# Optimization experiments

Hardware: AMD Instinct MI355X
Metric: run time of the kernel (lower is better)

## Reference

```python
import jax, jax.numpy as jnp
import numpy as np

REG = 0.1
EPS = 2.220446049250313e-16  # np.finfo(float).eps, cast to working dtype


def setup_inputs() -> dict:
    key = jax.random.key(0)
    k1, k2, k3 = jax.random.split(key, 3)
    x = jax.random.normal(k1, (262144, 512), dtype=jnp.float32)
    w = jax.random.normal(k2, (512,), dtype=jnp.float32)
    b = jax.random.normal(k3, (1,), dtype=jnp.float32)
    return {"x": x, "w": w, "b": b}


def reference(x, w, b):
    # net(x): [N, D] @ [D] + b -> [N]
    out = x @ w + b[0]
    n = out.shape[0]
    # sum(pdist(out[:, None], p=1)) == sum over i<j of |out_i - out_j|.
    # Exact sort-based closed form: with s sorted ascending,
    #   sum_{i<j}(s_j - s_i) = sum_i (2i - (n-1)) * s_i
    s = jnp.sort(out)
    coef = 2.0 * jnp.arange(n, dtype=out.dtype) - jnp.asarray(n - 1, out.dtype)
    pair_sum = jnp.sum(coef * s)
    loss = -jnp.sum(out) + (REG / n) * pair_sum
    # heaviside(out, zero_pos=True) = relu(sign(out + eps)); prod -> verified flag
    is_verified = jnp.prod(jax.nn.relu(jnp.sign(out + jnp.asarray(EPS, out.dtype))))
    return loss, is_verified
```

## Files before the change

### kernel.cpp

```cpp
#include <hip/hip_runtime.h>
#include <stdint.h>
#include <stddef.h>

#define NBINS 65536
#define EPSF 2.220446049250313e-16f
#define RTILE 4096

__device__ __forceinline__ uint32_t f2key(float f) {
    uint32_t u = __float_as_uint(f);
    return (u & 0x80000000u) ? ~u : (u | 0x80000000u);
}
__device__ __forceinline__ float key2f(uint32_t k) {
    uint32_t u = (k & 0x80000000u) ? (k ^ 0x80000000u) : ~k;
    return __uint_as_float(u);
}

__global__ __launch_bounds__(256) void gemv_kernel(
    const float* __restrict__ x, const float* __restrict__ w,
    const float* __restrict__ bptr, uint32_t* __restrict__ keys,
    uint32_t* __restrict__ hist, int N, int D,
    double* __restrict__ sum_out, int* __restrict__ bad_flag)
{
    __shared__ float4 w4s[512];
    const int tid = threadIdx.x;
    const int nf4 = D >> 2;
    const float4* w4g = (const float4*)w;
    for (int i = tid; i < nf4; i += 256) w4s[i] = w4g[i];
    __syncthreads();

    const int wave = tid >> 6, lane = tid & 63;
    const int gwave = blockIdx.x * 4 + wave;
    const int nwaves = gridDim.x * 4;
    const int rows_per = (N + nwaves - 1) / nwaves;
    const int r0 = gwave * rows_per;
    const int r1 = (r0 + rows_per < N) ? (r0 + rows_per) : N;
    const float b0 = bptr[0];

    double lsum = 0.0;
    int lbad = 0;
    for (int row = r0; row < r1; ++row) {
        const float4* xr = (const float4*)(x + (size_t)row * D);
        float dot = 0.f;
        for (int i = lane; i < nf4; i += 64) {
            float4 a = xr[i];
            float4 bb = w4s[i];
            dot = fmaf(a.x, bb.x, dot);
            dot = fmaf(a.y, bb.y, dot);
            dot = fmaf(a.z, bb.z, dot);
            dot = fmaf(a.w, bb.w, dot);
        }
        #pragma unroll
        for (int off = 32; off > 0; off >>= 1) dot += __shfl_down(dot, off, 64);
        if (lane == 0) {
            float f = dot + b0;
            uint32_t k = f2key(f);
            keys[row] = k;
            atomicAdd(&hist[k >> 16], 1u);
            lsum += (double)f;
            lbad |= (f + EPSF > 0.f) ? 0 : 1;
        }
    }

    __shared__ double sd[4];
    __shared__ int si[4];
    if (lane == 0) { sd[wave] = lsum; si[wave] = lbad; }
    __syncthreads();
    if (tid == 0) {
        atomicAdd(sum_out, sd[0] + sd[1] + sd[2] + sd[3]);
        int bd = si[0] | si[1] | si[2] | si[3];
        if (bd) atomicOr(bad_flag, 1);
    }
}

__global__ __launch_bounds__(1024) void scan_kernel(
    const uint32_t* __restrict__ hist, uint32_t* __restrict__ base,
    uint32_t* __restrict__ cnt, uint32_t* __restrict__ nzb,
    int* __restrict__ nb_count)
{
    __shared__ uint32_t partial[1024];
    __shared__ int nb_lds;
    const int t = threadIdx.x;
    if (t == 0) nb_lds = 0;
    const int per = NBINS / 1024;
    uint32_t s = 0;
    for (int i = 0; i < per; ++i) s += hist[t * per + i];
    partial[t] = s;
    __syncthreads();
    for (int off = 1; off < 1024; off <<= 1) {
        uint32_t v = (t >= off) ? partial[t - off] : 0u;
        __syncthreads();
        partial[t] += v;
        __syncthreads();
    }
    uint32_t run = (t == 0) ? 0u : partial[t - 1];
    for (int i = 0; i < per; ++i) {
        int idx = t * per + i;
        uint32_t h = hist[idx];
        base[idx] = run;
        cnt[idx] = run;
        if (h != 0u) {
            int pos = atomicAdd(&nb_lds, 1);
            nzb[pos] = (uint32_t)idx;
        }
        run += h;
    }
    if (t == 1023) base[NBINS] = run;
    __syncthreads();
    if (t == 0) *nb_count = nb_lds;
}

__global__ __launch_bounds__(256) void scatter_kernel(
    const uint32_t* __restrict__ keys, uint32_t* __restrict__ cnt,
    uint32_t* __restrict__ sorted, int N)
{
    int i = blockIdx.x * 256 + threadIdx.x;
    if (i < N) {
        uint32_t k = keys[i];
        uint32_t pos = atomicAdd(&cnt[k >> 16], 1u);
        sorted[pos] = k;
    }
}

__global__ __launch_bounds__(256) void rank_kernel(
    const uint32_t* __restrict__ sorted, const uint32_t* __restrict__ base,
    const uint32_t* __restrict__ nzb, const int* __restrict__ nb_count,
    int N, double* __restrict__ pair_acc, const double* __restrict__ sum_out,
    const int* __restrict__ bad_flag, int* __restrict__ done_cnt,
    float* __restrict__ out)
{
    __shared__ uint32_t tile[RTILE];
    __shared__ double sred[256];
    const int tid = threadIdx.x;
    const int nb = *nb_count;
    double acc = 0.0;

    for (int ib = blockIdx.x; ib < nb; ib += gridDim.x) {
        const uint32_t b = nzb[ib];
        const uint32_t start = base[b], end = base[b + 1];
        const uint32_t m = end - start;

        if (m <= RTILE) {
            __syncthreads();
            for (uint32_t j = tid; j < m; j += 256u) tile[j] = sorted[start + j];
            __syncthreads();
            const uint32_t rounds = (m + 255u) / 256u;
            for (uint32_t r = 0; r < rounds; ++r) {
                uint32_t p = r * 256u + (uint32_t)tid;
                if (p < m) {
                    uint32_t k = tile[p];
                    uint32_t lc = 0, eq = 0;
                    uint32_t m4 = m & ~3u, j = 0;
                    for (; j < m4; j += 4) {
                        uint4 t4 = *(const uint4*)(tile + j);
                        lc += (t4.x < k); eq += (t4.x == k);
                        lc += (t4.y < k); eq += (t4.y == k);
                        lc += (t4.z < k); eq += (t4.z == k);
                        lc += (t4.w < k); eq += (t4.w == k);
                    }
                    for (; j < m; ++j) {
                        uint32_t kk = tile[j];
                        lc += (kk < k); eq += (kk == k);
                    }
                    double coef = 2.0 * (double)(start + lc) + (double)eq - (double)N;
                    acc += coef * (double)key2f(k);
                }
            }
        } else {
            const uint32_t rounds = (m + 255u) / 256u;
            for (uint32_t r = 0; r < rounds; ++r) {
                uint32_t p = start + r * 256u + (uint32_t)tid;
                bool active = (p < end);
                uint32_t k = active ? sorted[p] : 0u;
                uint32_t lc = 0, eq = 0;
                for (uint32_t ts = start; ts < end; ts += RTILE) {
                    uint32_t tn = end - ts;
                    if (tn > RTILE) tn = RTILE;
                    __syncthreads();
                    for (uint32_t j = tid; j < tn; j += 256u) tile[j] = sorted[ts + j];
                    __syncthreads();
                    if (active) {
                        for (uint32_t j = 0; j < tn; ++j) {
                            uint32_t kk = tile[j];
                            lc += (kk < k); eq += (kk == k);
                        }
                    }
                }
                if (active) {
                    double coef = 2.0 * (double)(start + lc) + (double)eq - (double)N;
                    acc += coef * (double)key2f(k);
                }
            }
        }
    }

    sred[tid] = acc;
    __syncthreads();
    for (int off = 128; off > 0; off >>= 1) {
        if (tid < off) sred[tid] += sred[tid + off];
        __syncthreads();
    }
    if (tid == 0) {
        if (sred[0] != 0.0) atomicAdd(pair_acc, sred[0]);
        __threadfence();
        int d = atomicAdd(done_cnt, 1);
        if (d == (int)gridDim.x - 1) {
            __threadfence();
            double pp = __longlong_as_double(
                atomicAdd((unsigned long long*)pair_acc, 0ULL));
            double so = __longlong_as_double(
                atomicAdd((unsigned long long*)const_cast<double*>(sum_out), 0ULL));
            int bd = atomicAdd(const_cast<int*>(bad_flag), 0);
            double loss = -so + (0.1 / (double)N) * pp;
            out[0] = (float)loss;
            out[1] = bd ? 0.0f : 1.0f;
        }
    }
}

extern "C" void kernel_launch(void* const* d_in, const int* in_sizes, int n_in,
                              void* d_out, int out_size, void* d_ws, size_t ws_size,
                              hipStream_t stream) {
    (void)n_in; (void)out_size; (void)ws_size;
    const float* x = (const float*)d_in[0];
    const float* w = (const float*)d_in[1];
    const float* b = (const float*)d_in[2];
    float* out = (float*)d_out;
    const int D = in_sizes[1];
    const int N = in_sizes[0] / D;

    uint8_t* W = (uint8_t*)d_ws;
    uint32_t* hist     = (uint32_t*)(W);
    double*   sum_out  = (double*)(W + 262144);
    double*   pair_acc = (double*)(W + 262152);
    int*      bad_flag = (int*)(W + 262160);
    int*      done_cnt = (int*)(W + 262164);
    int*      nb_count = (int*)(W + 262168);
    uint32_t* base     = (uint32_t*)(W + 262176);
    uint32_t* cnt      = (uint32_t*)(W + 524336);
    uint32_t* nzb      = (uint32_t*)(W + 786480);
    uint32_t* keys     = (uint32_t*)(W + 1048624);
    uint32_t* sorted   = keys + N;

    hipMemsetAsync(d_ws, 0, 262176, stream);
    gemv_kernel<<<2048, 256, 0, stream>>>(x, w, b, keys, hist, N, D, sum_out, bad_flag);
    scan_kernel<<<1, 1024, 0, stream>>>(hist, base, cnt, nzb, nb_count);
    scatter_kernel<<<(N + 255) / 256, 256, 0, stream>>>(keys, cnt, sorted, N);
    rank_kernel<<<2048, 256, 0, stream>>>(sorted, base, nzb, nb_count, N,
                                          pair_acc, sum_out, bad_flag, done_cnt, out);
}
```

Baseline: 985.5 us.

## Parallelize histogram scan across 256 blocks using coarse top-byte counts

The gemv kernel now also builds a 256-bin coarse histogram on the top key byte, kept in shared memory and flushed with global atomics. The single-block 1024-thread scan over 65536 bins is replaced by 256 blocks. Each block gets its base offset by reducing the coarse counts below it, then scans its own 256 fine bins. This removes a serial single-CU bottleneck, at the cost of extra LDS and global atomics in the gemv, and the nonzero-bin list now comes out in nondeterministic order.

```diff
diff --git a/kernel.cpp b/kernel.cpp
--- a/kernel.cpp
+++ b/kernel.cpp
@@ -18,14 +18,16 @@
 __global__ __launch_bounds__(256) void gemv_kernel(
     const float* __restrict__ x, const float* __restrict__ w,
     const float* __restrict__ bptr, uint32_t* __restrict__ keys,
-    uint32_t* __restrict__ hist, int N, int D,
-    double* __restrict__ sum_out, int* __restrict__ bad_flag)
+    uint32_t* __restrict__ hist, uint32_t* __restrict__ coarse,
+    int N, int D, double* __restrict__ sum_out, int* __restrict__ bad_flag)
 {
     __shared__ float4 w4s[512];
+    __shared__ uint32_t ch[256];
     const int tid = threadIdx.x;
     const int nf4 = D >> 2;
     const float4* w4g = (const float4*)w;
     for (int i = tid; i < nf4; i += 256) w4s[i] = w4g[i];
+    ch[tid] = 0u;
     __syncthreads();
 
     const int wave = tid >> 6, lane = tid & 63;
@@ -56,6 +58,7 @@
             uint32_t k = f2key(f);
             keys[row] = k;
             atomicAdd(&hist[k >> 16], 1u);
+            atomicAdd(&ch[k >> 24], 1u);
             lsum += (double)f;
             lbad |= (f + EPSF > 0.f) ? 0 : 1;
         }
@@ -65,6 +68,7 @@
     __shared__ int si[4];
     if (lane == 0) { sd[wave] = lsum; si[wave] = lbad; }
     __syncthreads();
+    if (ch[tid]) atomicAdd(&coarse[tid], ch[tid]);
     if (tid == 0) {
         atomicAdd(sum_out, sd[0] + sd[1] + sd[2] + sd[3]);
         int bd = si[0] | si[1] | si[2] | si[3];
@@ -72,41 +76,42 @@
     }
 }
 
-__global__ __launch_bounds__(1024) void scan_kernel(
-    const uint32_t* __restrict__ hist, uint32_t* __restrict__ base,
-    uint32_t* __restrict__ cnt, uint32_t* __restrict__ nzb,
-    int* __restrict__ nb_count)
-{
-    __shared__ uint32_t partial[1024];
-    __shared__ int nb_lds;
+__global__ __launch_bounds__(256) void scan_kernel(
+    const uint32_t* __restrict__ hist, const uint32_t* __restrict__ coarse,
+    uint32_t* __restrict__ base, uint32_t* __restrict__ cnt,
+    uint32_t* __restrict__ nzb, int* __restrict__ nb_count)
+{
+    __shared__ uint32_t red[256];
+    __shared__ uint32_t s[256];
     const int t = threadIdx.x;
-    if (t == 0) nb_lds = 0;
-    const int per = NBINS / 1024;
-    uint32_t s = 0;
-    for (int i = 0; i < per; ++i) s += hist[t * per + i];
-    partial[t] = s;
-    __syncthreads();
-    for (int off = 1; off < 1024; off <<= 1) {
-        uint32_t v = (t >= off) ? partial[t - off] : 0u;
-        __syncthreads();
-        partial[t] += v;
-        __syncthreads();
-    }
-    uint32_t run = (t == 0) ? 0u : partial[t - 1];
-    for (int i = 0; i < per; ++i) {
-        int idx = t * per + i;
-        uint32_t h = hist[idx];
-        base[idx] = run;
-        cnt[idx] = run;
-        if (h != 0u) {
-            int pos = atomicAdd(&nb_lds, 1);
-            nzb[pos] = (uint32_t)idx;
-        }
-        run += h;
-    }
-    if (t == 1023) base[NBINS] = run;
-    __syncthreads();
-    if (t == 0) *nb_count = nb_lds;
+    const int j = blockIdx.x;
+    const int g = j * 256 + t;
+
+    red[t] = (t < j) ? coarse[t] : 0u;
+    __syncthreads();
+    for (int off = 128; off > 0; off >>= 1) {
+        if (t < off) red[t] += red[t + off];
+        __syncthreads();
+    }
+    const uint32_t cb = red[0];
+
+    const uint32_t h = hist[g];
+    s[t] = h;
+    __syncthreads();
+    for (int off = 1; off < 256; off <<= 1) {
+        uint32_t v = (t >= off) ? s[t - off] : 0u;
+        __syncthreads();
+        s[t] += v;
+        __syncthreads();
+    }
+    const uint32_t excl = cb + s[t] - h;
+    base[g] = excl;
+    cnt[g] = excl;
+    if (h) {
+        int pos = atomicAdd(nb_count, 1);
+        nzb[pos] = (uint32_t)g;
+    }
+    if (g == NBINS - 1) base[NBINS] = excl + h;
 }
 
 __global__ __launch_bounds__(256) void scatter_kernel(
@@ -230,20 +235,22 @@
 
     uint8_t* W = (uint8_t*)d_ws;
     uint32_t* hist     = (uint32_t*)(W);
-    double*   sum_out  = (double*)(W + 262144);
-    double*   pair_acc = (double*)(W + 262152);
-    int*      bad_flag = (int*)(W + 262160);
-    int*      done_cnt = (int*)(W + 262164);
-    int*      nb_count = (int*)(W + 262168);
-    uint32_t* base     = (uint32_t*)(W + 262176);
-    uint32_t* cnt      = (uint32_t*)(W + 524336);
-    uint32_t* nzb      = (uint32_t*)(W + 786480);
-    uint32_t* keys     = (uint32_t*)(W + 1048624);
+    uint32_t* coarse   = (uint32_t*)(W + 262144);
+    double*   sum_out  = (double*)(W + 263168);
+    double*   pair_acc = (double*)(W + 263176);
+    int*      bad_flag = (int*)(W + 263184);
+    int*      done_cnt = (int*)(W + 263188);
+    int*      nb_count = (int*)(W + 263192);
+    uint32_t* base     = (uint32_t*)(W + 263200);
+    uint32_t* cnt      = (uint32_t*)(W + 525352);
+    uint32_t* nzb      = (uint32_t*)(W + 787496);
+    uint32_t* keys     = (uint32_t*)(W + 1049640);
     uint32_t* sorted   = keys + N;
 
-    hipMemsetAsync(d_ws, 0, 262176, stream);
-    gemv_kernel<<<2048, 256, 0, stream>>>(x, w, b, keys, hist, N, D, sum_out, bad_flag);
-    scan_kernel<<<1, 1024, 0, stream>>>(hist, base, cnt, nzb, nb_count);
+    hipMemsetAsync(d_ws, 0, 263200, stream);
+    gemv_kernel<<<2048, 256, 0, stream>>>(x, w, b, keys, hist, coarse, N, D,
+                                          sum_out, bad_flag);
+    scan_kernel<<<256, 256, 0, stream>>>(hist, coarse, base, cnt, nzb, nb_count);
     scatter_kernel<<<(N + 255) / 256, 256, 0, stream>>>(keys, cnt, sorted, N);
     rank_kernel<<<2048, 256, 0, stream>>>(sorted, base, nzb, nb_count, N,
                                           pair_acc, sum_out, bad_flag, done_cnt, out);
```

Measured after the change: 841.7 us. 1.17x faster.
